# Kernel optimization log

Measured on AMD Instinct MI355X. Metric: run time of the kernel, lower is better.

Reference implementation:

```python
import jax, jax.numpy as jnp
import numpy as np

N, E, D, H, L = 4096, 131072, 2048, 4, 2  # nodes, edges, embed_dim, heads, layers
HD = D // H


def setup_inputs() -> dict:
    key = jax.random.key(0)
    ks = jax.random.split(key, 11)
    s = 0.02
    feats = jax.random.normal(ks[0], (N, D), jnp.float32)
    edge_index = jax.random.randint(ks[1], (E, 2), 0, N, dtype=jnp.int32)
    # per-layer linear params, stored as [in, out] so y = x @ W + b (== torch x @ W.T + b)
    Wq = jax.random.normal(ks[2], (L, D, D), jnp.float32) * s
    Wk = jax.random.normal(ks[3], (L, D, D), jnp.float32) * s
    Wv = jax.random.normal(ks[4], (L, D, D), jnp.float32) * s
    Wo = jax.random.normal(ks[5], (L, D, D), jnp.float32) * s
    bq = jnp.zeros((L, D), jnp.float32)
    bk = jnp.zeros((L, D), jnp.float32)
    bv = jnp.zeros((L, D), jnp.float32)
    bo = jnp.zeros((L, D), jnp.float32)
    return dict(feats=feats, Wq=Wq, bq=bq, Wk=Wk, bk=bk, Wv=Wv, bv=bv,
                Wo=Wo, bo=bo, edge_index=edge_index)


def _gnn_forward(feats, Wq, bq, Wk, bk, Wv, bv, Wo, bo, row, col):
    n = feats.shape[0]
    # dense edge mask [1, N, N] (masked_fill where mask == 0 -> -10000)
    mask = jnp.zeros((n, n), bool).at[row, col].set(True)[None]
    scale = 1.0 / jnp.sqrt(jnp.asarray(HD, feats.dtype))
    x = feats
    for l in range(L):
        q = (x @ Wq[l] + bq[l]).reshape(n, H, HD).transpose(1, 0, 2)  # [H,N,d]
        k = (x @ Wk[l] + bk[l]).reshape(n, H, HD).transpose(1, 0, 2)
        v = (x @ Wv[l] + bv[l]).reshape(n, H, HD).transpose(1, 0, 2)
        scores = jnp.einsum('hnd,hmd->hnm', q, k) * scale          # [H,N,N]
        scores = jnp.where(mask, scores, jnp.asarray(-10000.0, scores.dtype))
        attn = jax.nn.softmax(scores, axis=-1)                      # [H,N,N]
        se = attn[:, row, col]                                      # [H,E] gather per-edge
        out_e = se[:, :, None] * v[:, col]                          # [H,E,d]
        agg = jax.vmap(lambda o: jax.ops.segment_sum(o, row, num_segments=n))(out_e)  # [H,N,d]
        x = agg.transpose(1, 0, 2).reshape(n, H * HD) @ Wo[l] + bo[l]
    return x


def reference(feats, Wq, bq, Wk, bk, Wv, bv, Wo, bo, edge_index):
    row, col = edge_index[:, 0], edge_index[:, 1]
    return _gnn_forward(feats, Wq, bq, Wk, bk, Wv, bv, Wo, bo, row, col)
```

## Files before the change

### kernel.cpp

```cpp
#include <hip/hip_runtime.h>
#include <hip/hip_bf16.h>

typedef unsigned short u16;
typedef unsigned int u32;
typedef short bf16x8 __attribute__((ext_vector_type(8)));
typedef float f32x4 __attribute__((ext_vector_type(4)));
typedef unsigned short u16x4 __attribute__((ext_vector_type(4)));
typedef unsigned short u16x8 __attribute__((ext_vector_type(8)));
typedef float f32x4v __attribute__((ext_vector_type(4)));

#define NN 4096
#define DD 2048
#define HH 4
#define HDIM 512
#define EE 131072
#define NB 512
#define EBS 256
#define QS 6144

__device__ __forceinline__ float bf2f(u16 x) {
    return __uint_as_float(((u32)x) << 16);
}
__device__ __forceinline__ u16 f2bf(float f) {
    u32 u = __float_as_uint(f);
    u += 0x7fffu + ((u >> 16) & 1u);
    return (u16)(u >> 16);
}

#define GLOAD16(g, l)                                                          \
    __builtin_amdgcn_global_load_lds(                                          \
        (const __attribute__((address_space(1))) void*)(g),                    \
        (__attribute__((address_space(3))) void*)(l), 16, 0, 0)

__global__ __launch_bounds__(256) void k_cvt(const float* __restrict__ in,
                                             u16* __restrict__ out, int n4)
{
    int i = blockIdx.x * 256 + threadIdx.x;
    if (i >= n4) return;
    f32x4v v = *(const f32x4v*)&in[i * 4];
    u16x4 o;
#pragma unroll
    for (int j = 0; j < 4; j++) o[j] = f2bf(v[j]);
    *(u16x4*)&out[i * 4] = o;
}

template <bool OUTF32>
__global__ __launch_bounds__(256, 2) void k_gemm(
    const u16* __restrict__ A, const u16* __restrict__ Bt,
    const float* __restrict__ bias0, const float* __restrict__ bias1,
    const float* __restrict__ bias2, void* __restrict__ Cout,
    int M, int Ncols, int K)
{
    extern __shared__ u16 lds[];
    u16* sA = lds;
    u16* sB = lds + 3 * 8192;

    int t = threadIdx.x;
    int wid = t >> 6, lane = t & 63;
    int wr = wid >> 1, wc = wid & 1;
    int l15 = lane & 15, kg = lane >> 4;

    int flat = blockIdx.y * gridDim.x + blockIdx.x;
    int per = (gridDim.x * gridDim.y) >> 3;
    int nid = (flat & 7) * per + (flat >> 3);
    int gy = gridDim.y;
    int bm = nid % gy;
    int bn = nid / gy;

    const int NT = K >> 5;

    int trow = t >> 2;
    int scolE = ((t & 3) ^ ((t >> 3) & 3)) * 8;
    const u16* Abase = A + ((size_t)bm * 256 + trow) * K + scolE;
    const u16* Bbase = Bt + ((size_t)bn * 128 + trow) * K + scolE;

#define STAGE_A(buf, TT, j)                                                    \
    GLOAD16(Abase + (size_t)(j) * 64 * K + (size_t)(TT) * 32,                  \
            sA + (buf) * 8192 + (j) * 2048 + t * 8)
#define STAGE_B(buf, TT, j)                                                    \
    GLOAD16(Bbase + (size_t)(j) * 64 * K + (size_t)(TT) * 32,                  \
            sB + (buf) * 4096 + (j) * 2048 + t * 8)

    int sl = (kg ^ ((l15 >> 1) & 3)) * 8;

    f32x4 acc[8][4];
#pragma unroll
    for (int m = 0; m < 8; m++)
#pragma unroll
        for (int n = 0; n < 4; n++) acc[m][n] = (f32x4){0.f, 0.f, 0.f, 0.f};

#pragma unroll
    for (int j = 0; j < 4; j++) STAGE_A(0, 0, j);
    STAGE_B(0, 0, 0); STAGE_B(0, 0, 1);
#pragma unroll
    for (int j = 0; j < 4; j++) STAGE_A(1, 1, j);
    STAGE_B(1, 1, 0); STAGE_B(1, 1, 1);
    asm volatile("s_waitcnt vmcnt(6)" ::: "memory");
    __builtin_amdgcn_s_barrier();

    int bufc = 0;
    for (int T = 0; T < NT; ++T) {
        const u16* bA = sA + bufc * 8192;
        const u16* bB = sB + bufc * 4096;
        int nxt2 = bufc + 2; if (nxt2 >= 3) nxt2 -= 3;
        if (T + 2 < NT) {
#pragma unroll
            for (int j = 0; j < 4; j++) STAGE_A(nxt2, T + 2, j);
            STAGE_B(nxt2, T + 2, 0); STAGE_B(nxt2, T + 2, 1);
        }
        bf16x8 bfr[4], afr[8];
#pragma unroll
        for (int n = 0; n < 4; ++n)
            bfr[n] = *(const bf16x8*)(bB + (wc * 64 + n * 16 + l15) * 32 + sl);
#pragma unroll
        for (int m = 0; m < 8; ++m)
            afr[m] = *(const bf16x8*)(bA + (wr * 128 + m * 16 + l15) * 32 + sl);
        __builtin_amdgcn_s_setprio(1);
#pragma unroll
        for (int m = 0; m < 8; ++m)
#pragma unroll
            for (int n = 0; n < 4; ++n)
                acc[m][n] = __builtin_amdgcn_mfma_f32_16x16x32_bf16(
                    afr[m], bfr[n], acc[m][n], 0, 0, 0);
        __builtin_amdgcn_s_setprio(0);
        if (T + 2 < NT)
            asm volatile("s_waitcnt vmcnt(6)" ::: "memory");
        else if (T + 1 < NT)
            asm volatile("s_waitcnt vmcnt(0)" ::: "memory");
        __builtin_amdgcn_s_barrier();
        bufc += 1; if (bufc >= 3) bufc -= 3;
    }
#undef STAGE_A
#undef STAGE_B

    int row0 = bm * 256 + wr * 128 + kg * 4;
    int col0 = bn * 128 + wc * 64 + l15;
#pragma unroll
    for (int n = 0; n < 4; n++) {
        int cc = col0 + n * 16;
        int sel = cc >> 11;
        const float* bp = (sel == 0) ? bias0 : (sel == 1) ? bias1 : bias2;
        float bv = bp[cc & 2047];
#pragma unroll
        for (int m = 0; m < 8; m++) {
            int rb = row0 + m * 16;
#pragma unroll
            for (int r = 0; r < 4; r++) {
                float v = acc[m][n][r] + bv;
                if (OUTF32)
                    ((float*)Cout)[(size_t)(rb + r) * Ncols + cc] = v;
                else
                    ((u16*)Cout)[(size_t)(rb + r) * Ncols + cc] = f2bf(v);
            }
        }
    }
}

__global__ void k_wtrans(const float* __restrict__ Wq, const float* __restrict__ Wk,
                         const float* __restrict__ Wv, const float* __restrict__ Wo,
                         int loff, u16* __restrict__ Wt)
{
    int z = blockIdx.z;
    const float* W = (z == 0) ? Wq : (z == 1) ? Wk : (z == 2) ? Wv : Wo;
    u16* out = Wt + (size_t)z * DD * DD;
    __shared__ u16 tile[32][33];
    int tx = threadIdx.x, ty = threadIdx.y;
    int x = blockIdx.x * 32 + tx;
    int y0 = blockIdx.y * 32;
#pragma unroll
    for (int j = 0; j < 32; j += 8)
        tile[ty + j][tx] = f2bf(W[loff + (size_t)(y0 + ty + j) * DD + x]);
    __syncthreads();
    int ox = blockIdx.y * 32 + tx;
    int oy0 = blockIdx.x * 32;
#pragma unroll
    for (int j = 0; j < 32; j += 8)
        out[(size_t)(oy0 + ty + j) * DD + ox] = tile[tx][ty + j];
}

__global__ __launch_bounds__(256) void k_hist(const int* __restrict__ ei,
                                              int* __restrict__ blockcnt)
{
    __shared__ int h[NN];
    int b = blockIdx.x, t = threadIdx.x;
    for (int i = t; i < NN; i += 256) h[i] = 0;
    __syncthreads();
    int2 e = ((const int2*)ei)[b * EBS + t];
    atomicAdd(&h[e.x], 1);
    __syncthreads();
    for (int i = t; i < NN; i += 256) blockcnt[(size_t)b * NN + i] = h[i];
}

__global__ void k_rowscan(int* __restrict__ blockcnt, int* __restrict__ rowsum)
{
    int i = blockIdx.x * 256 + threadIdx.x;
    int run = 0;
    for (int b = 0; b < NB; b++) {
        int v = blockcnt[(size_t)b * NN + i];
        blockcnt[(size_t)b * NN + i] = run;
        run += v;
    }
    rowsum[i] = run;
}

__global__ __launch_bounds__(1024) void k_scan2(const int* __restrict__ rowsum,
                                                int* __restrict__ rstart)
{
    __shared__ int sh[1024];
    int t = threadIdx.x;
    int v[4], pre[4], s = 0;
#pragma unroll
    for (int j = 0; j < 4; j++) v[j] = rowsum[t * 4 + j];
#pragma unroll
    for (int j = 0; j < 4; j++) { pre[j] = s; s += v[j]; }
    sh[t] = s;
    __syncthreads();
    for (int off = 1; off < 1024; off <<= 1) {
        int x = (t >= off) ? sh[t - off] : 0;
        __syncthreads();
        sh[t] += x;
        __syncthreads();
    }
    int bp = (t == 0) ? 0 : sh[t - 1];
#pragma unroll
    for (int j = 0; j < 4; j++) rstart[t * 4 + j] = bp + pre[j];
    if (t == 1023) rstart[NN] = sh[1023];
}

__global__ __launch_bounds__(256) void k_scatter2(
    const int* __restrict__ ei, const int* __restrict__ blockcnt,
    const int* __restrict__ rstart, int* __restrict__ srow,
    int* __restrict__ scol)
{
    __shared__ int rsh[EBS];
    int b = blockIdx.x, t = threadIdx.x;
    int2 e = ((const int2*)ei)[b * EBS + t];
    rsh[t] = e.x;
    __syncthreads();
    int rank = 0;
    for (int j = 0; j < t; j++) rank += (rsh[j] == e.x);
    int pos = rstart[e.x] + blockcnt[(size_t)b * NN + e.x] + rank;
    srow[pos] = e.x;
    scol[pos] = e.y;
}

__global__ __launch_bounds__(64) void k_flags(const int* __restrict__ scol,
                                              const int* __restrict__ rstart,
                                              int* __restrict__ flags)
{
    int i = blockIdx.x;
    int start = rstart[i], end = rstart[i + 1];
    int d = end - start;
    __shared__ int sc[1024];
    int lane = threadIdx.x;
    for (int j = lane; j < d && j < 1024; j += 64) sc[j] = scol[start + j];
    __syncthreads();
    for (int j = lane; j < d; j += 64) {
        int cj = (j < 1024) ? sc[j] : scol[start + j];
        int f = 1;
        for (int q = 0; q < j; ++q) {
            int cq = (q < 1024) ? sc[q] : scol[start + q];
            if (cq == cj) { f = 0; break; }
        }
        flags[start + j] = f;
    }
}

__global__ __launch_bounds__(256) void k_scores(
    const u16* __restrict__ Qb, const u16* __restrict__ Kb,
    const int* __restrict__ srow, const int* __restrict__ scol,
    float* __restrict__ pexp)
{
    int p = blockIdx.x * 4 + (threadIdx.x >> 6);
    int lane = threadIdx.x & 63;
    int h = lane >> 4, l16 = lane & 15;
    int r = srow[p], c = scol[p];
    const float scale = 0.04419417382415922f;
    const u16* qrow = Qb + (size_t)r * QS + h * HDIM + l16 * 8;
    const u16* krow = Kb + (size_t)c * QS + h * HDIM + l16 * 8;
    float sx = 0.f, sy = 0.f;
#pragma unroll
    for (int ch = 0; ch < 4; ++ch) {
        u16x8 q8 = *(const u16x8*)(qrow + ch * 128);
        u16x8 k8 = *(const u16x8*)(krow + ch * 128);
#pragma unroll
        for (int j = 0; j < 8; j += 2) {
            sx += bf2f(q8[j]) * bf2f(k8[j]);
            sy += bf2f(q8[j + 1]) * bf2f(k8[j + 1]);
        }
    }
    float s = sx + sy;
#pragma unroll
    for (int off = 1; off < 16; off <<= 1) s += __shfl_xor(s, off, 64);
    if (l16 == 0) pexp[p * 4 + h] = expf(s * scale);
}

__global__ __launch_bounds__(256) void k_agg(
    const float* __restrict__ pexp, const int* __restrict__ flags,
    const int* __restrict__ scol, const int* __restrict__ rstart,
    const u16* __restrict__ Vb, u16* __restrict__ Aggb)
{
    int i = blockIdx.x;
    int start = rstart[i], end = rstart[i + 1];
    int h = threadIdx.x >> 6, lane = threadIdx.x & 63;
    __shared__ float sden[HH];
    float dsum = 0.f;
    for (int p = start + lane; p < end; p += 64)
        if (flags[p]) dsum += pexp[p * 4 + h];
#pragma unroll
    for (int off = 32; off > 0; off >>= 1) dsum += __shfl_xor(dsum, off, 64);
    if (lane == 0) sden[h] = dsum;
    __syncthreads();
    float inv = (end > start) ? 1.0f / sden[h] : 0.0f;
    float acc[8] = {0.f, 0.f, 0.f, 0.f, 0.f, 0.f, 0.f, 0.f};
    for (int p = start; p < end; ++p) {
        float wgt = pexp[p * 4 + h] * inv;
        int c = scol[p];
        u16x8 v8 = *(const u16x8*)&Vb[(size_t)c * QS + h * HDIM + lane * 8];
#pragma unroll
        for (int j = 0; j < 8; j++) acc[j] += wgt * bf2f(v8[j]);
    }
    u16x8 o;
#pragma unroll
    for (int j = 0; j < 8; j++) o[j] = f2bf(acc[j]);
    *(u16x8*)&Aggb[(size_t)i * DD + h * HDIM + lane * 8] = o;
}

extern "C" void kernel_launch(void* const* d_in, const int* in_sizes, int n_in,
                              void* d_out, int out_size, void* d_ws, size_t ws_size,
                              hipStream_t stream)
{
    const float* feats = (const float*)d_in[0];
    const float* Wq = (const float*)d_in[1];
    const float* bq = (const float*)d_in[2];
    const float* Wk = (const float*)d_in[3];
    const float* bk = (const float*)d_in[4];
    const float* Wv = (const float*)d_in[5];
    const float* bv = (const float*)d_in[6];
    const float* Wo = (const float*)d_in[7];
    const float* bo = (const float*)d_in[8];
    const int* ei = (const int*)d_in[9];
    float* out = (float*)d_out;

    size_t off = 0;
    auto alloc = [&](size_t bytes) {
        void* p = (char*)d_ws + off;
        off += (bytes + 255) & ~(size_t)255;
        return p;
    };
    const size_t ND = (size_t)NN * DD;
    u16* Xb = (u16*)alloc(ND * 2);
    u16* QKV = (u16*)alloc((size_t)NN * QS * 2);
    u16* Ab = (u16*)alloc(ND * 2);
    u16* Wt = (u16*)alloc((size_t)4 * DD * DD * 2);
    float* pexp = (float*)alloc((size_t)EE * HH * 4);
    int* blockcnt = (int*)alloc((size_t)NB * NN * 4);
    int* rowsum = (int*)alloc((size_t)NN * 4);
    int* rstart = (int*)alloc((size_t)(NN + 1) * 4);
    int* srow = (int*)alloc((size_t)EE * 4);
    int* scol = (int*)alloc((size_t)EE * 4);
    int* flags = (int*)alloc((size_t)EE * 4);
    (void)ws_size; (void)in_sizes; (void)n_in; (void)out_size;

    const int GEMM_LDS = 3 * (8192 + 4096) * 2;
    hipFuncSetAttribute((const void*)k_gemm<false>,
                        hipFuncAttributeMaxDynamicSharedMemorySize, GEMM_LDS);
    hipFuncSetAttribute((const void*)k_gemm<true>,
                        hipFuncAttributeMaxDynamicSharedMemorySize, GEMM_LDS);

    k_hist<<<NB, 256, 0, stream>>>(ei, blockcnt);
    k_rowscan<<<NN / 256, 256, 0, stream>>>(blockcnt, rowsum);
    k_scan2<<<1, 1024, 0, stream>>>(rowsum, rstart);
    k_scatter2<<<NB, 256, 0, stream>>>(ei, blockcnt, rstart, srow, scol);
    k_flags<<<NN, 64, 0, stream>>>(scol, rstart, flags);

    k_cvt<<<(int)(ND / 4 / 256), 256, 0, stream>>>(feats, Xb, (int)(ND / 4));

    dim3 gqkv(QS / 128, NN / 256);
    dim3 go(DD / 128, NN / 256);
    for (int l = 0; l < 2; ++l) {
        k_wtrans<<<dim3(DD / 32, DD / 32, 4), dim3(32, 8), 0, stream>>>(
            Wq, Wk, Wv, Wo, l * DD * DD, Wt);
        k_gemm<false><<<gqkv, 256, GEMM_LDS, stream>>>(
            Xb, Wt, bq + l * DD, bk + l * DD, bv + l * DD, QKV, NN, QS, DD);
        k_scores<<<EE / 4, 256, 0, stream>>>(QKV, QKV + DD, srow, scol, pexp);
        k_agg<<<NN, 256, 0, stream>>>(pexp, flags, scol, rstart, QKV + 2 * DD, Ab);
        if (l == 1) {
            k_gemm<true><<<go, 256, GEMM_LDS, stream>>>(
                Ab, Wt + 3 * (size_t)DD * DD, bo + l * DD, bo + l * DD, bo + l * DD, out, NN, DD, DD);
        } else {
            k_gemm<false><<<go, 256, GEMM_LDS, stream>>>(
                Ab, Wt + 3 * (size_t)DD * DD, bo + l * DD, bo + l * DD, bo + l * DD, Xb, NN, DD, DD);
        }
    }
}
```

Before: 688.4 us.

## Load GEMM B fragments directly from global into registers, drop B LDS staging

The GEMM kernel stops staging B tiles through shared memory. Each wave now loads its B fragments straight from global memory into registers, double-buffered one k-step ahead, and only A keeps the triple-buffered LDS pipeline. This removes the B LDS traffic and halves the shared memory footprint, which may allow more resident blocks. In exchange, the two row-wise waves sharing a column half now load the same B data from global, with small per-lane 16-byte loads that are less coalesced, and register pressure rises.

```diff
diff --git a/kernel.cpp b/kernel.cpp
--- a/kernel.cpp
+++ b/kernel.cpp
@@ -51,9 +51,7 @@
     const float* __restrict__ bias2, void* __restrict__ Cout,
     int M, int Ncols, int K)
 {
-    extern __shared__ u16 lds[];
-    u16* sA = lds;
-    u16* sB = lds + 3 * 8192;
+    __shared__ u16 sA[3 * 8192];
 
     int t = threadIdx.x;
     int wid = t >> 6, lane = t & 63;
@@ -72,14 +70,18 @@
     int trow = t >> 2;
     int scolE = ((t & 3) ^ ((t >> 3) & 3)) * 8;
     const u16* Abase = A + ((size_t)bm * 256 + trow) * K + scolE;
-    const u16* Bbase = Bt + ((size_t)bn * 128 + trow) * K + scolE;
 
 #define STAGE_A(buf, TT, j)                                                    \
     GLOAD16(Abase + (size_t)(j) * 64 * K + (size_t)(TT) * 32,                  \
             sA + (buf) * 8192 + (j) * 2048 + t * 8)
-#define STAGE_B(buf, TT, j)                                                    \
-    GLOAD16(Bbase + (size_t)(j) * 64 * K + (size_t)(TT) * 32,                  \
-            sB + (buf) * 4096 + (j) * 2048 + t * 8)
+
+    const u16* Bwav = Bt + ((size_t)bn * 128 + wc * 64 + l15) * K + kg * 8;
+#define LOADB(dst, TT)                                                         \
+    {                                                                          \
+        _Pragma("unroll")                                                      \
+        for (int n = 0; n < 4; ++n)                                            \
+            dst[n] = *(const bf16x8*)(Bwav + (size_t)(n * 16) * K + (TT) * 32);\
+    }
 
     int sl = (kg ^ ((l15 >> 1) & 3)) * 8;
 
@@ -89,29 +91,26 @@
 #pragma unroll
         for (int n = 0; n < 4; n++) acc[m][n] = (f32x4){0.f, 0.f, 0.f, 0.f};
 
+    bf16x8 bcur[4], bnxt[4];
+
+    LOADB(bcur, 0);
 #pragma unroll
     for (int j = 0; j < 4; j++) STAGE_A(0, 0, j);
-    STAGE_B(0, 0, 0); STAGE_B(0, 0, 1);
 #pragma unroll
     for (int j = 0; j < 4; j++) STAGE_A(1, 1, j);
-    STAGE_B(1, 1, 0); STAGE_B(1, 1, 1);
-    asm volatile("s_waitcnt vmcnt(6)" ::: "memory");
+    asm volatile("s_waitcnt vmcnt(4)" ::: "memory");
     __builtin_amdgcn_s_barrier();
 
     int bufc = 0;
     for (int T = 0; T < NT; ++T) {
         const u16* bA = sA + bufc * 8192;
-        const u16* bB = sB + bufc * 4096;
         int nxt2 = bufc + 2; if (nxt2 >= 3) nxt2 -= 3;
+        if (T + 1 < NT) LOADB(bnxt, T + 1);
         if (T + 2 < NT) {
 #pragma unroll
             for (int j = 0; j < 4; j++) STAGE_A(nxt2, T + 2, j);
-            STAGE_B(nxt2, T + 2, 0); STAGE_B(nxt2, T + 2, 1);
-        }
-        bf16x8 bfr[4], afr[8];
-#pragma unroll
-        for (int n = 0; n < 4; ++n)
-            bfr[n] = *(const bf16x8*)(bB + (wc * 64 + n * 16 + l15) * 32 + sl);
+        }
+        bf16x8 afr[8];
 #pragma unroll
         for (int m = 0; m < 8; ++m)
             afr[m] = *(const bf16x8*)(bA + (wr * 128 + m * 16 + l15) * 32 + sl);
@@ -121,17 +120,21 @@
 #pragma unroll
             for (int n = 0; n < 4; ++n)
                 acc[m][n] = __builtin_amdgcn_mfma_f32_16x16x32_bf16(
-                    afr[m], bfr[n], acc[m][n], 0, 0, 0);
+                    afr[m], bcur[n], acc[m][n], 0, 0, 0);
         __builtin_amdgcn_s_setprio(0);
+        if (T + 1 < NT) {
+#pragma unroll
+            for (int n = 0; n < 4; ++n) bcur[n] = bnxt[n];
+        }
         if (T + 2 < NT)
-            asm volatile("s_waitcnt vmcnt(6)" ::: "memory");
+            asm volatile("s_waitcnt vmcnt(4)" ::: "memory");
         else if (T + 1 < NT)
             asm volatile("s_waitcnt vmcnt(0)" ::: "memory");
-        __builtin_amdgcn_s_barrier();
+        if (T + 1 < NT) __builtin_amdgcn_s_barrier();
         bufc += 1; if (bufc >= 3) bufc -= 3;
     }
 #undef STAGE_A
-#undef STAGE_B
+#undef LOADB
 
     int row0 = bm * 256 + wr * 128 + kg * 4;
     int col0 = bn * 128 + wc * 64 + l15;
@@ -362,12 +365,6 @@
     int* flags = (int*)alloc((size_t)EE * 4);
     (void)ws_size; (void)in_sizes; (void)n_in; (void)out_size;
 
-    const int GEMM_LDS = 3 * (8192 + 4096) * 2;
-    hipFuncSetAttribute((const void*)k_gemm<false>,
-                        hipFuncAttributeMaxDynamicSharedMemorySize, GEMM_LDS);
-    hipFuncSetAttribute((const void*)k_gemm<true>,
-                        hipFuncAttributeMaxDynamicSharedMemorySize, GEMM_LDS);
-
     k_hist<<<NB, 256, 0, stream>>>(ei, blockcnt);
     k_rowscan<<<NN / 256, 256, 0, stream>>>(blockcnt, rowsum);
     k_scan2<<<1, 1024, 0, stream>>>(rowsum, rstart);
@@ -381,15 +378,15 @@
     for (int l = 0; l < 2; ++l) {
         k_wtrans<<<dim3(DD / 32, DD / 32, 4), dim3(32, 8), 0, stream>>>(
             Wq, Wk, Wv, Wo, l * DD * DD, Wt);
-        k_gemm<false><<<gqkv, 256, GEMM_LDS, stream>>>(
+        k_gemm<false><<<gqkv, 256, 0, stream>>>(
             Xb, Wt, bq + l * DD, bk + l * DD, bv + l * DD, QKV, NN, QS, DD);
         k_scores<<<EE / 4, 256, 0, stream>>>(QKV, QKV + DD, srow, scol, pexp);
         k_agg<<<NN, 256, 0, stream>>>(pexp, flags, scol, rstart, QKV + 2 * DD, Ab);
         if (l == 1) {
-            k_gemm<true><<<go, 256, GEMM_LDS, stream>>>(
+            k_gemm<true><<<go, 256, 0, stream>>>(
                 Ab, Wt + 3 * (size_t)DD * DD, bo + l * DD, bo + l * DD, bo + l * DD, out, NN, DD, DD);
         } else {
-            k_gemm<false><<<go, 256, GEMM_LDS, stream>>>(
+            k_gemm<false><<<go, 256, 0, stream>>>(
                 Ab, Wt + 3 * (size_t)DD * DD, bo + l * DD, bo + l * DD, bo + l * DD, Xb, NN, DD, DD);
         }
     }
```

Result: slower. 897.7 us (+30.4%).

## Fuse edge score and aggregation kernels into one per-row edge kernel

Applied to the files above, without the earlier changes.

Replaces the separate per-edge score kernel and the per-row aggregation kernel with a single per-row kernel. It holds the row's Q in registers, computes exp-scores into LDS, normalises, then aggregates V with a 2-way unrolled loop. This removes the global pexp round trip and the repeated Q loads, at the cost of lower parallelism in the score phase. Degree is clamped to MAXDEG=256, which silently truncates rows with more edges.

```diff
diff --git a/kernel.cpp b/kernel.cpp
--- a/kernel.cpp
+++ b/kernel.cpp
@@ -17,6 +17,7 @@
 #define NB 512
 #define EBS 256
 #define QS 6144
+#define MAXDEG 256
 
 __device__ __forceinline__ float bf2f(u16 x) {
     return __uint_as_float(((u32)x) << 16);
@@ -266,64 +267,89 @@
     }
 }
 
-__global__ __launch_bounds__(256) void k_scores(
-    const u16* __restrict__ Qb, const u16* __restrict__ Kb,
-    const int* __restrict__ srow, const int* __restrict__ scol,
-    float* __restrict__ pexp)
-{
-    int p = blockIdx.x * 4 + (threadIdx.x >> 6);
-    int lane = threadIdx.x & 63;
-    int h = lane >> 4, l16 = lane & 15;
-    int r = srow[p], c = scol[p];
-    const float scale = 0.04419417382415922f;
-    const u16* qrow = Qb + (size_t)r * QS + h * HDIM + l16 * 8;
-    const u16* krow = Kb + (size_t)c * QS + h * HDIM + l16 * 8;
-    float sx = 0.f, sy = 0.f;
-#pragma unroll
-    for (int ch = 0; ch < 4; ++ch) {
-        u16x8 q8 = *(const u16x8*)(qrow + ch * 128);
-        u16x8 k8 = *(const u16x8*)(krow + ch * 128);
-#pragma unroll
-        for (int j = 0; j < 8; j += 2) {
-            sx += bf2f(q8[j]) * bf2f(k8[j]);
-            sy += bf2f(q8[j + 1]) * bf2f(k8[j + 1]);
-        }
-    }
-    float s = sx + sy;
-#pragma unroll
-    for (int off = 1; off < 16; off <<= 1) s += __shfl_xor(s, off, 64);
-    if (l16 == 0) pexp[p * 4 + h] = expf(s * scale);
-}
-
-__global__ __launch_bounds__(256) void k_agg(
-    const float* __restrict__ pexp, const int* __restrict__ flags,
-    const int* __restrict__ scol, const int* __restrict__ rstart,
-    const u16* __restrict__ Vb, u16* __restrict__ Aggb)
+__global__ __launch_bounds__(256) void k_edge(
+    const u16* __restrict__ QKV, const int* __restrict__ scol,
+    const int* __restrict__ flags, const int* __restrict__ rstart,
+    u16* __restrict__ Aggb)
 {
     int i = blockIdx.x;
     int start = rstart[i], end = rstart[i + 1];
-    int h = threadIdx.x >> 6, lane = threadIdx.x & 63;
-    __shared__ float sden[HH];
-    float dsum = 0.f;
-    for (int p = start + lane; p < end; p += 64)
-        if (flags[p]) dsum += pexp[p * 4 + h];
-#pragma unroll
-    for (int off = 32; off > 0; off >>= 1) dsum += __shfl_xor(dsum, off, 64);
-    if (lane == 0) sden[h] = dsum;
-    __syncthreads();
-    float inv = (end > start) ? 1.0f / sden[h] : 0.0f;
+    int deg = end - start;
+    if (deg > MAXDEG) deg = MAXDEG;
+    int t = threadIdx.x;
+    int wid = t >> 6, lane = t & 63;
+    int h = lane >> 4, l16 = lane & 15;
+
+    __shared__ float pexpS[MAXDEG * HH];
+    __shared__ float sinv[HH];
+    __shared__ int scolS[MAXDEG];
+
+    for (int j = t; j < deg; j += 256) scolS[j] = scol[start + j];
+
+    const u16* qrow = QKV + (size_t)i * QS + h * HDIM + l16 * 8;
+    u16x8 qreg[4];
+#pragma unroll
+    for (int ch = 0; ch < 4; ++ch) qreg[ch] = *(const u16x8*)(qrow + ch * 128);
+    __syncthreads();
+
+    const float scale = 0.04419417382415922f;
+
+    for (int j = wid; j < deg; j += 4) {
+        int c = scolS[j];
+        const u16* krow = QKV + (size_t)c * QS + DD + h * HDIM + l16 * 8;
+        float sx = 0.f, sy = 0.f;
+#pragma unroll
+        for (int ch = 0; ch < 4; ++ch) {
+            u16x8 k8 = *(const u16x8*)(krow + ch * 128);
+#pragma unroll
+            for (int jj = 0; jj < 8; jj += 2) {
+                sx += bf2f(qreg[ch][jj]) * bf2f(k8[jj]);
+                sy += bf2f(qreg[ch][jj + 1]) * bf2f(k8[jj + 1]);
+            }
+        }
+        float s = sx + sy;
+#pragma unroll
+        for (int off = 1; off < 16; off <<= 1) s += __shfl_xor(s, off, 64);
+        if (l16 == 0) pexpS[j * HH + h] = expf(s * scale);
+    }
+    __syncthreads();
+
+    {
+        float dsum = 0.f;
+        for (int j = lane; j < deg; j += 64)
+            if (flags[start + j]) dsum += pexpS[j * HH + wid];
+#pragma unroll
+        for (int off = 32; off > 0; off >>= 1) dsum += __shfl_xor(dsum, off, 64);
+        if (lane == 0) sinv[wid] = (deg > 0) ? 1.0f / dsum : 0.0f;
+    }
+    __syncthreads();
+
+    float inv = sinv[wid];
     float acc[8] = {0.f, 0.f, 0.f, 0.f, 0.f, 0.f, 0.f, 0.f};
-    for (int p = start; p < end; ++p) {
-        float wgt = pexp[p * 4 + h] * inv;
-        int c = scol[p];
-        u16x8 v8 = *(const u16x8*)&Vb[(size_t)c * QS + h * HDIM + lane * 8];
-#pragma unroll
-        for (int j = 0; j < 8; j++) acc[j] += wgt * bf2f(v8[j]);
+    const u16* Vcol = QKV + 2 * DD + wid * HDIM + lane * 8;
+    int j = 0;
+    for (; j + 2 <= deg; j += 2) {
+        int c0 = scolS[j], c1 = scolS[j + 1];
+        u16x8 v0 = *(const u16x8*)(Vcol + (size_t)c0 * QS);
+        u16x8 v1 = *(const u16x8*)(Vcol + (size_t)c1 * QS);
+        float w0 = pexpS[j * HH + wid] * inv;
+        float w1 = pexpS[(j + 1) * HH + wid] * inv;
+#pragma unroll
+        for (int e = 0; e < 8; e++) acc[e] += w0 * bf2f(v0[e]);
+#pragma unroll
+        for (int e = 0; e < 8; e++) acc[e] += w1 * bf2f(v1[e]);
+    }
+    if (j < deg) {
+        int c0 = scolS[j];
+        u16x8 v0 = *(const u16x8*)(Vcol + (size_t)c0 * QS);
+        float w0 = pexpS[j * HH + wid] * inv;
+#pragma unroll
+        for (int e = 0; e < 8; e++) acc[e] += w0 * bf2f(v0[e]);
     }
     u16x8 o;
 #pragma unroll
-    for (int j = 0; j < 8; j++) o[j] = f2bf(acc[j]);
-    *(u16x8*)&Aggb[(size_t)i * DD + h * HDIM + lane * 8] = o;
+    for (int e = 0; e < 8; e++) o[e] = f2bf(acc[e]);
+    *(u16x8*)&Aggb[(size_t)i * DD + wid * HDIM + lane * 8] = o;
 }
 
 extern "C" void kernel_launch(void* const* d_in, const int* in_sizes, int n_in,
@@ -353,7 +379,6 @@
     u16* QKV = (u16*)alloc((size_t)NN * QS * 2);
     u16* Ab = (u16*)alloc(ND * 2);
     u16* Wt = (u16*)alloc((size_t)4 * DD * DD * 2);
-    float* pexp = (float*)alloc((size_t)EE * HH * 4);
     int* blockcnt = (int*)alloc((size_t)NB * NN * 4);
     int* rowsum = (int*)alloc((size_t)NN * 4);
     int* rstart = (int*)alloc((size_t)(NN + 1) * 4);
@@ -383,8 +408,7 @@
             Wq, Wk, Wv, Wo, l * DD * DD, Wt);
         k_gemm<false><<<gqkv, 256, GEMM_LDS, stream>>>(
             Xb, Wt, bq + l * DD, bk + l * DD, bv + l * DD, QKV, NN, QS, DD);
-        k_scores<<<EE / 4, 256, 0, stream>>>(QKV, QKV + DD, srow, scol, pexp);
-        k_agg<<<NN, 256, 0, stream>>>(pexp, flags, scol, rstart, QKV + 2 * DD, Ab);
+        k_edge<<<NN, 256, 0, stream>>>(QKV, scol, flags, rstart, Ab);
         if (l == 1) {
             k_gemm<true><<<go, 256, GEMM_LDS, stream>>>(
                 Ab, Wt + 3 * (size_t)DD * DD, bo + l * DD, bo + l * DD, bo + l * DD, out, NN, DD, DD);
```

Result: no change. 678.2 us (-1.5%).
